# Kernel optimization log

Measured on AMD Instinct MI355X. Metric: run time of the kernel, lower is better.

Reference implementation:

```python
import jax, jax.numpy as jnp
import numpy as np

NEG_BIG = 1e13  # matches the torch module's (mask-1)*1e13 additive mask


def setup_inputs() -> dict:
    key = jax.random.key(0)
    k1, k2, k3, k4 = jax.random.split(key, 4)
    B, Lq, Lk, D = 32, 1024, 1024, 1024  # D = 2*hidden = 2*embedding
    query = jax.random.normal(k1, (B, Lq, D), dtype=jnp.float32)
    key_t = jax.random.normal(k2, (B, Lk, D), dtype=jnp.float32)
    key_mask = jax.random.randint(k3, (B, Lk), 0, 2).astype(jnp.float32)
    # Linear(hidden*2 -> embedding*2): weight [out, in] torch convention
    W = jax.random.normal(k4, (D, D), dtype=jnp.float32) * (1.0 / np.sqrt(D))
    b = jnp.zeros((D,), dtype=jnp.float32)
    return {"query": query, "key": key_t, "key_mask": key_mask, "W": W, "b": b}


def reference(query, key, key_mask, W, b):
    # query_emb: Dropout (identity at eval) -> Linear -> ReLU
    query_feat = jax.nn.relu(jnp.einsum("bqd,ed->bqe", query, W) + b)  # [B,Lq,D]
    # bmm with multiplicatively masked key
    masked_key = key * key_mask[:, :, None]                             # [B,Lk,D]
    score = jnp.einsum("bqd,bkd->bqk", query_feat, masked_key)          # [B,Lq,Lk]
    # masked_softmax: score*mask + (mask-1)*1e13, softmax over last dim
    m = key_mask[:, None, :]                                            # [B,1,Lk]
    attn = jax.nn.softmax(score * m + (m - 1.0) * NEG_BIG, axis=-1)     # [B,Lq,Lk]
    # weighted sum over the UNmasked key (as in the original module)
    return jnp.einsum("bqk,bkd->bqd", attn, key)                        # [B,Lq,D]
```

## Files before the change

### kernel.cpp

```cpp
#include <hip/hip_runtime.h>
#include <hip/hip_bf16.h>


typedef __attribute__((ext_vector_type(4))) float f32x4;
typedef __attribute__((ext_vector_type(8))) short s16x8;

#define MFMA16(a, b, c) __builtin_amdgcn_mfma_f32_16x16x32_bf16((a), (b), (c), 0, 0, 0)

__device__ __forceinline__ unsigned short f2bf(float x) {
  unsigned u = __builtin_bit_cast(unsigned, x);
  return (unsigned short)((u + 0x7FFFu + ((u >> 16) & 1u)) >> 16);
}
__device__ __forceinline__ float bf2f(unsigned short h) {
  return __builtin_bit_cast(float, ((unsigned)h) << 16);
}
__device__ __forceinline__ int swz(int row, int col) {
  return (row * 64 + col) ^ ((row & 7) << 3);
}
__device__ __forceinline__ void cvt8(const float* __restrict__ s, s16x8& h8, s16x8& l8) {
  f32x4 a = *(const f32x4*)s;
  f32x4 b = *(const f32x4*)(s + 4);
#pragma unroll
  for (int i = 0; i < 8; i++) {
    float v = (i < 4) ? a[i] : b[i - 4];
    unsigned short hu = f2bf(v);
    unsigned short lu = f2bf(v - bf2f(hu));
    h8[i] = (short)hu;
    l8[i] = (short)lu;
  }
}
__device__ __forceinline__ void gld16(const void* g, void* lds) {
  __builtin_amdgcn_global_load_lds((const __attribute__((address_space(1))) unsigned int*)g,
                                   (__attribute__((address_space(3))) unsigned int*)lds, 16, 0, 0);
}

#define OFF_KHI 0ULL
#define OFF_KLO 67108864ULL
#define OFF_KHIT 134217728ULL
#define OFF_QHI 201326592ULL
#define OFF_QLO 268435456ULL
#define OFF_WHI 335544320ULL
#define OFF_WLO 337641472ULL
#define WS_TIER_A 339738624ULL
#define WS_TIER_B2 201326592ULL

__global__ __launch_bounds__(256) void k_cvt_pair(const float* __restrict__ src,
                                                  unsigned short* __restrict__ hi,
                                                  unsigned short* __restrict__ lo, int n8) {
  int i = blockIdx.x * 256 + threadIdx.x;
  if (i >= n8) return;
  s16x8 h, l;
  cvt8(src + (size_t)i * 8, h, l);
  *(s16x8*)(hi + (size_t)i * 8) = h;
  *(s16x8*)(lo + (size_t)i * 8) = l;
}

__global__ __launch_bounds__(256) void k_cvt_k(const float* __restrict__ K,
                                               unsigned short* __restrict__ Khi,
                                               unsigned short* __restrict__ Klo,
                                               unsigned short* __restrict__ KhiT) {
  __shared__ unsigned T[64 * 65];
  const int t = threadIdx.x;
  const int db0 = blockIdx.x * 64, kb0 = blockIdx.y * 64, b = blockIdx.z;
  const size_t base = (size_t)b * 1024 * 1024;
#pragma unroll
  for (int i = 0; i < 2; i++) {
    const int r = (t >> 3) + i * 32, c0 = (t & 7) * 8;
    s16x8 h, l;
    cvt8(K + base + (size_t)(kb0 + r) * 1024 + db0 + c0, h, l);
    *(s16x8*)(Khi + base + (size_t)(kb0 + r) * 1024 + db0 + c0) = h;
    *(s16x8*)(Klo + base + (size_t)(kb0 + r) * 1024 + db0 + c0) = l;
#pragma unroll
    for (int j = 0; j < 8; j++)
      T[r * 65 + c0 + j] = ((unsigned)(unsigned short)h[j] << 16) | (unsigned short)l[j];
  }
  __syncthreads();
#pragma unroll
  for (int i = 0; i < 2; i++) {
    const int rd = (t >> 3) + i * 32, ck0 = (t & 7) * 8;
    s16x8 h;
#pragma unroll
    for (int j = 0; j < 8; j++) h[j] = (short)(unsigned short)(T[(ck0 + j) * 65 + rd] >> 16);
    *(s16x8*)(KhiT + base + (size_t)(db0 + rd) * 1024 + kb0 + ck0) = h;
  }
}

__global__ __launch_bounds__(256, 2) void k_qf2(const unsigned short* __restrict__ Qhi,
                                                const unsigned short* __restrict__ Qlo,
                                                const unsigned short* __restrict__ Whi,
                                                const unsigned short* __restrict__ Wlo,
                                                const float* __restrict__ bias,
                                                float* __restrict__ outp) {
  __shared__ __align__(16) unsigned short Ah[128 * 64], Al[128 * 64], Bh[128 * 64], Bl[128 * 64];
  const int t = threadIdx.x;
  const int i = blockIdx.x + blockIdx.y * 256;
  const int x = i & 7, j = i >> 3;
  const int n0 = (j & 7) * 128;
  const int m0 = (x * 32 + (j >> 3)) * 128;
  const int w = t >> 6, l = t & 63, wm = w >> 1, wn = w & 1, g = l >> 4, ln = l & 15;
  const int lrow = l >> 3, lc8 = (l & 7) * 8;
  const f32x4 fz = {0.f, 0.f, 0.f, 0.f};
  f32x4 acc[4][4];
#pragma unroll
  for (int a = 0; a < 4; a++)
#pragma unroll
    for (int bq = 0; bq < 4; bq++) acc[a][bq] = fz;
#pragma unroll 1
  for (int k0 = 0; k0 < 1024; k0 += 64) {
#pragma unroll
    for (int jj = 0; jj < 4; jj++) {
      const int ch = w * 4 + jj;
      const int row = ch * 8 + lrow;
      const int sc = lc8 ^ (lrow << 3);
      gld16(Qhi + (size_t)(m0 + row) * 1024 + k0 + sc, &Ah[ch * 512]);
      gld16(Qlo + (size_t)(m0 + row) * 1024 + k0 + sc, &Al[ch * 512]);
      gld16(Whi + (size_t)(n0 + row) * 1024 + k0 + sc, &Bh[ch * 512]);
      gld16(Wlo + (size_t)(n0 + row) * 1024 + k0 + sc, &Bl[ch * 512]);
    }
    __syncthreads();
#pragma unroll
    for (int ks = 0; ks < 2; ks++) {
      const int kc = ks * 32 + g * 8;
      s16x8 ah[4], al[4], bh[4], bl[4];
#pragma unroll
      for (int mf = 0; mf < 4; mf++) {
        const int row = wm * 64 + mf * 16 + ln;
        const int idx = row * 64 + (kc ^ ((row & 7) << 3));
        ah[mf] = *(const s16x8*)&Ah[idx];
        al[mf] = *(const s16x8*)&Al[idx];
      }
#pragma unroll
      for (int nf = 0; nf < 4; nf++) {
        const int row = wn * 64 + nf * 16 + ln;
        const int idx = row * 64 + (kc ^ ((row & 7) << 3));
        bh[nf] = *(const s16x8*)&Bh[idx];
        bl[nf] = *(const s16x8*)&Bl[idx];
      }
#pragma unroll
      for (int mf = 0; mf < 4; mf++)
#pragma unroll
        for (int nf = 0; nf < 4; nf++) {
          acc[mf][nf] = MFMA16(ah[mf], bh[nf], acc[mf][nf]);
          acc[mf][nf] = MFMA16(ah[mf], bl[nf], acc[mf][nf]);
          acc[mf][nf] = MFMA16(al[mf], bh[nf], acc[mf][nf]);
        }
    }
    __syncthreads();
  }
  unsigned short* oc = (unsigned short*)outp;
#pragma unroll
  for (int nf = 0; nf < 4; nf++) {
    const int col = n0 + wn * 64 + nf * 16 + ln;
    const float bv = bias[col];
#pragma unroll
    for (int mf = 0; mf < 4; mf++)
#pragma unroll
      for (int r = 0; r < 4; r++) {
        const int row = m0 + wm * 64 + mf * 16 + g * 4 + r;
        float v = acc[mf][nf][r] + bv;
        v = v > 0.f ? v : 0.f;
        unsigned short h = f2bf(v);
        oc[(size_t)row * 2048 + col] = h;
        oc[(size_t)row * 2048 + 1024 + col] = f2bf(v - bf2f(h));
      }
  }
}

__global__ __launch_bounds__(512, 2) void k_attn2(const unsigned short* __restrict__ Khi,
                                                  const unsigned short* __restrict__ Klo,
                                                  const float* __restrict__ mask,
                                                  float* __restrict__ dout) {
  __shared__ __align__(16) unsigned short kbuf[2][2][128 * 64];
  __shared__ float mask_s[1024];
  __shared__ float red[4][64];
  const int t = threadIdx.x;
  const int i = blockIdx.y * 16 + blockIdx.x;
  const int x = i & 7, jj = i >> 3;
  const int b = x * 4 + (jj >> 4), qt = jj & 15;
  const int q0 = qt * 64;
  const int w = t >> 6, l = t & 63, wm = w >> 2, wn = w & 3, g = l >> 4, ln = l & 15;
  const int lrow = l >> 3, lc8 = (l & 7) * 8, sc = lc8 ^ (lrow << 3);
  for (int ii = t; ii < 1024; ii += 512) mask_s[ii] = mask[b * 1024 + ii];
  const f32x4 fz = {0.f, 0.f, 0.f, 0.f};
  f32x4 acc[8][2][2];
#pragma unroll
  for (int kt = 0; kt < 8; kt++)
#pragma unroll
    for (int mf = 0; mf < 2; mf++)
#pragma unroll
      for (int nf = 0; nf < 2; nf++) acc[kt][mf][nf] = fz;
  const unsigned short* dou16 = (const unsigned short*)dout;
  const size_t kbase = (size_t)b * 1024 * 1024;

  auto stageK = [&](int buf, int kt, int dc) {
#pragma unroll
    for (int jj2 = 0; jj2 < 2; jj2++) {
      const int ch = w * 2 + jj2;
      const int row = ch * 8 + lrow;
      const size_t go = kbase + (size_t)(kt * 128 + row) * 1024 + dc * 64 + sc;
      gld16(Khi + go, &kbuf[buf][0][ch * 512]);
      gld16(Klo + go, &kbuf[buf][1][ch * 512]);
    }
  };

  stageK(0, 0, 0);
  __syncthreads();
  int cur = 0;
#pragma unroll 1
  for (int dc = 0; dc < 16; dc++) {
    s16x8 qh[2][2], ql[2][2];
#pragma unroll
    for (int mf = 0; mf < 2; mf++)
#pragma unroll
      for (int ks = 0; ks < 2; ks++) {
        const size_t rowoff = (size_t)(b * 1024 + q0 + wm * 32 + mf * 16 + ln) * 2048;
        const int col = dc * 64 + ks * 32 + g * 8;
        qh[mf][ks] = *(const s16x8*)(dou16 + rowoff + col);
        ql[mf][ks] = *(const s16x8*)(dou16 + rowoff + 1024 + col);
      }
#pragma unroll
    for (int kt = 0; kt < 8; kt++) {
      if (!(dc == 15 && kt == 7)) {
        const int nkt = (kt + 1) & 7;
        const int ndc = (kt == 7) ? dc + 1 : dc;
        stageK(cur ^ 1, nkt, ndc);
      }
#pragma unroll
      for (int ks = 0; ks < 2; ks++) {
        const int kc = ks * 32 + g * 8;
        s16x8 bh[2], bl[2];
#pragma unroll
        for (int nf = 0; nf < 2; nf++) {
          const int row = wn * 32 + nf * 16 + ln;
          const int idx = row * 64 + (kc ^ ((row & 7) << 3));
          bh[nf] = *(const s16x8*)&kbuf[cur][0][idx];
          bl[nf] = *(const s16x8*)&kbuf[cur][1][idx];
        }
#pragma unroll
        for (int mf = 0; mf < 2; mf++)
#pragma unroll
          for (int nf = 0; nf < 2; nf++) {
            acc[kt][mf][nf] = MFMA16(qh[mf][ks], bh[nf], acc[kt][mf][nf]);
            acc[kt][mf][nf] = MFMA16(qh[mf][ks], bl[nf], acc[kt][mf][nf]);
            acc[kt][mf][nf] = MFMA16(ql[mf][ks], bh[nf], acc[kt][mf][nf]);
          }
      }
      __syncthreads();
      cur ^= 1;
    }
  }
  float rmax[2][4];
#pragma unroll
  for (int mf = 0; mf < 2; mf++)
#pragma unroll
    for (int r = 0; r < 4; r++) rmax[mf][r] = -1e30f;
#pragma unroll
  for (int kt = 0; kt < 8; kt++)
#pragma unroll
    for (int nf = 0; nf < 2; nf++) {
      const int k = kt * 128 + wn * 32 + nf * 16 + ln;
      const bool mk = mask_s[k] != 0.f;
#pragma unroll
      for (int mf = 0; mf < 2; mf++)
#pragma unroll
        for (int r = 0; r < 4; r++)
          if (mk) rmax[mf][r] = fmaxf(rmax[mf][r], acc[kt][mf][nf][r]);
    }
#pragma unroll
  for (int off = 1; off < 16; off <<= 1)
#pragma unroll
    for (int mf = 0; mf < 2; mf++)
#pragma unroll
      for (int r = 0; r < 4; r++) rmax[mf][r] = fmaxf(rmax[mf][r], __shfl_xor(rmax[mf][r], off));
  if (ln == 0) {
#pragma unroll
    for (int mf = 0; mf < 2; mf++)
#pragma unroll
      for (int r = 0; r < 4; r++) red[wn][wm * 32 + mf * 16 + g * 4 + r] = rmax[mf][r];
  }
  __syncthreads();
#pragma unroll
  for (int mf = 0; mf < 2; mf++)
#pragma unroll
    for (int r = 0; r < 4; r++) {
      const int row = wm * 32 + mf * 16 + g * 4 + r;
      rmax[mf][r] = fmaxf(fmaxf(red[0][row], red[1][row]), fmaxf(red[2][row], red[3][row]));
    }
  __syncthreads();
  float rsum[2][4];
#pragma unroll
  for (int mf = 0; mf < 2; mf++)
#pragma unroll
    for (int r = 0; r < 4; r++) rsum[mf][r] = 0.f;
#pragma unroll
  for (int kt = 0; kt < 8; kt++)
#pragma unroll
    for (int nf = 0; nf < 2; nf++) {
      const int k = kt * 128 + wn * 32 + nf * 16 + ln;
      const bool mk = mask_s[k] != 0.f;
#pragma unroll
      for (int mf = 0; mf < 2; mf++)
#pragma unroll
        for (int r = 0; r < 4; r++)
          if (mk) rsum[mf][r] += __expf(acc[kt][mf][nf][r] - rmax[mf][r]);
    }
#pragma unroll
  for (int off = 1; off < 16; off <<= 1)
#pragma unroll
    for (int mf = 0; mf < 2; mf++)
#pragma unroll
      for (int r = 0; r < 4; r++) rsum[mf][r] += __shfl_xor(rsum[mf][r], off);
  if (ln == 0) {
#pragma unroll
    for (int mf = 0; mf < 2; mf++)
#pragma unroll
      for (int r = 0; r < 4; r++) red[wn][wm * 32 + mf * 16 + g * 4 + r] = rsum[mf][r];
  }
  __syncthreads();
  float rinv[2][4];
#pragma unroll
  for (int mf = 0; mf < 2; mf++)
#pragma unroll
    for (int r = 0; r < 4; r++) {
      const int row = wm * 32 + mf * 16 + g * 4 + r;
      rinv[mf][r] = 1.f / (red[0][row] + red[1][row] + red[2][row] + red[3][row]);
    }
  unsigned short* oc = (unsigned short*)dout;
#pragma unroll
  for (int kt = 0; kt < 8; kt++)
#pragma unroll
    for (int nf = 0; nf < 2; nf++) {
      const int k = kt * 128 + wn * 32 + nf * 16 + ln;
      const bool mk = mask_s[k] != 0.f;
#pragma unroll
      for (int mf = 0; mf < 2; mf++)
#pragma unroll
        for (int r = 0; r < 4; r++) {
          const int q = q0 + wm * 32 + mf * 16 + g * 4 + r;
          float p = mk ? __expf(acc[kt][mf][nf][r] - rmax[mf][r]) * rinv[mf][r] : 0.f;
          oc[(size_t)(b * 1024 + q) * 2048 + 1024 + k] = f2bf(p);
        }
    }
}

__global__ __launch_bounds__(512, 2) void k_pv2(const unsigned short* __restrict__ KhiT,
                                                float* __restrict__ dout, const int dh) {
  __shared__ __align__(16) unsigned short P[128 * 64];
  __shared__ __align__(16) unsigned short KT[512 * 64];
  const int t = threadIdx.x;
  const int i = blockIdx.y * 8 + blockIdx.x;
  const int x = i & 7, jj = i >> 3;
  const int b = x * 4 + (jj >> 3), qt = jj & 7;
  const int q0 = qt * 128, d0 = dh * 512;
  const int w = t >> 6, l = t & 63, wm = w >> 2, wd = w & 3, g = l >> 4, ln = l & 15;
  const int lrow = l >> 3, lc8 = (l & 7) * 8, sc = lc8 ^ (lrow << 3);
  const f32x4 fz = {0.f, 0.f, 0.f, 0.f};
  f32x4 acc[4][8];
#pragma unroll
  for (int a = 0; a < 4; a++)
#pragma unroll
    for (int bq = 0; bq < 8; bq++) acc[a][bq] = fz;
  const unsigned short* dou16 = (const unsigned short*)dout;
  const size_t kbase = (size_t)b * 1024 * 1024;
#pragma unroll 1
  for (int k0 = 0; k0 < 1024; k0 += 64) {
#pragma unroll
    for (int jj2 = 0; jj2 < 2; jj2++) {
      const int ch = w * 2 + jj2;
      const int row = ch * 8 + lrow;
      gld16(dou16 + (size_t)(b * 1024 + q0 + row) * 2048 + 1024 + k0 + sc, &P[ch * 512]);
    }
#pragma unroll
    for (int jj2 = 0; jj2 < 8; jj2++) {
      const int ch = w * 8 + jj2;
      const int row = ch * 8 + lrow;
      gld16(KhiT + kbase + (size_t)(d0 + row) * 1024 + k0 + sc, &KT[ch * 512]);
    }
    __syncthreads();
#pragma unroll
    for (int ks = 0; ks < 2; ks++) {
      const int kc = ks * 32 + g * 8;
      s16x8 a[4], bb[8];
#pragma unroll
      for (int mf = 0; mf < 4; mf++) {
        const int row = wm * 64 + mf * 16 + ln;
        a[mf] = *(const s16x8*)&P[row * 64 + (kc ^ ((row & 7) << 3))];
      }
#pragma unroll
      for (int nf = 0; nf < 8; nf++) {
        const int row = wd * 128 + nf * 16 + ln;
        bb[nf] = *(const s16x8*)&KT[row * 64 + (kc ^ ((row & 7) << 3))];
      }
#pragma unroll
      for (int mf = 0; mf < 4; mf++)
#pragma unroll
        for (int nf = 0; nf < 8; nf++) acc[mf][nf] = MFMA16(a[mf], bb[nf], acc[mf][nf]);
    }
    __syncthreads();
  }
#pragma unroll
  for (int mf = 0; mf < 4; mf++)
#pragma unroll
    for (int nf = 0; nf < 8; nf++)
#pragma unroll
      for (int r = 0; r < 4; r++) {
        const int q = q0 + wm * 64 + mf * 16 + g * 4 + r;
        const int d = d0 + wd * 128 + nf * 16 + ln;
        dout[(size_t)(b * 1024 + q) * 1024 + d] = acc[mf][nf][r];
      }
}

__global__ __launch_bounds__(256, 2) void k_qf(const float* __restrict__ Q,
                                               const float* __restrict__ W,
                                               const float* __restrict__ bias,
                                               float* __restrict__ qf, const int packout) {
  __shared__ __align__(16) short Ah[128 * 64], Al[128 * 64], Bh[128 * 64], Bl[128 * 64];
  const int t = threadIdx.x;
  const int m0 = blockIdx.x * 128, n0 = blockIdx.y * 128;
  const int w = t >> 6, l = t & 63, wm = w >> 1, wn = w & 1, g = l >> 4, ln = l & 15;
  const f32x4 fz = {0.f, 0.f, 0.f, 0.f};
  f32x4 acc[4][4];
#pragma unroll
  for (int a = 0; a < 4; a++)
#pragma unroll
    for (int bq = 0; bq < 4; bq++) acc[a][bq] = fz;
  const int srow = t >> 1, scol = (t & 1) * 32;
#pragma unroll 1
  for (int k0 = 0; k0 < 1024; k0 += 64) {
    const float* sa = Q + (size_t)(m0 + srow) * 1024 + k0 + scol;
    const float* sb = W + (size_t)(n0 + srow) * 1024 + k0 + scol;
#pragma unroll
    for (int c = 0; c < 32; c += 8) {
      s16x8 h, lo;
      cvt8(sa + c, h, lo);
      int si = swz(srow, scol + c);
      *(s16x8*)&Ah[si] = h;
      *(s16x8*)&Al[si] = lo;
    }
#pragma unroll
    for (int c = 0; c < 32; c += 8) {
      s16x8 h, lo;
      cvt8(sb + c, h, lo);
      int si = swz(srow, scol + c);
      *(s16x8*)&Bh[si] = h;
      *(s16x8*)&Bl[si] = lo;
    }
    __syncthreads();
#pragma unroll
    for (int ks = 0; ks < 2; ks++) {
      const int kc = ks * 32 + g * 8;
      s16x8 ah[4], al[4], bh[4], bl[4];
#pragma unroll
      for (int mf = 0; mf < 4; mf++) {
        int si = swz(wm * 64 + mf * 16 + ln, kc);
        ah[mf] = *(s16x8*)&Ah[si];
        al[mf] = *(s16x8*)&Al[si];
      }
#pragma unroll
      for (int nf = 0; nf < 4; nf++) {
        int si = swz(wn * 64 + nf * 16 + ln, kc);
        bh[nf] = *(s16x8*)&Bh[si];
        bl[nf] = *(s16x8*)&Bl[si];
      }
#pragma unroll
      for (int mf = 0; mf < 4; mf++)
#pragma unroll
        for (int nf = 0; nf < 4; nf++) {
          acc[mf][nf] = MFMA16(ah[mf], bh[nf], acc[mf][nf]);
          acc[mf][nf] = MFMA16(ah[mf], bl[nf], acc[mf][nf]);
          acc[mf][nf] = MFMA16(al[mf], bh[nf], acc[mf][nf]);
        }
    }
    __syncthreads();
  }
  unsigned short* oc = (unsigned short*)qf;
#pragma unroll
  for (int nf = 0; nf < 4; nf++) {
    const int col = n0 + wn * 64 + nf * 16 + ln;
    const float bv = bias[col];
#pragma unroll
    for (int mf = 0; mf < 4; mf++)
#pragma unroll
      for (int r = 0; r < 4; r++) {
        const int row = m0 + wm * 64 + mf * 16 + g * 4 + r;
        float v = acc[mf][nf][r] + bv;
        v = v > 0.f ? v : 0.f;
        if (packout) {
          unsigned short h = f2bf(v);
          oc[(size_t)row * 2048 + col] = h;
          oc[(size_t)row * 2048 + 1024 + col] = f2bf(v - bf2f(h));
        } else {
          qf[(size_t)row * 1024 + col] = v;
        }
      }
  }
}

__global__ __launch_bounds__(512, 2) void k_attn(const float* __restrict__ Key,
                                                 const float* __restrict__ mask,
                                                 float* __restrict__ dout) {
  __shared__ __align__(16) short qh[64 * 64], qlo[64 * 64], kh[128 * 64], klo[128 * 64];
  __shared__ float mask_s[1024];
  __shared__ float red[4][64];
  const int t = threadIdx.x;
  const int qt = blockIdx.x, b = blockIdx.y;
  const int q0 = qt * 64;
  const int w = t >> 6, l = t & 63, wm = w >> 2, wn = w & 3, g = l >> 4, ln = l & 15;
  for (int i = t; i < 1024; i += 512) mask_s[i] = mask[b * 1024 + i];
  const f32x4 fz = {0.f, 0.f, 0.f, 0.f};
  f32x4 acc[8][2][2];
#pragma unroll
  for (int kt = 0; kt < 8; kt++)
#pragma unroll
    for (int mf = 0; mf < 2; mf++)
#pragma unroll
      for (int nf = 0; nf < 2; nf++) acc[kt][mf][nf] = fz;
  const float* qfb = dout + (size_t)(b * 1024 + q0) * 1024;
  const float* kb = Key + (size_t)b * 1024 * 1024;
  const int qrow = t >> 3, qcol = (t & 7) * 8;
  const int krow = t >> 2, kcol0 = (t & 3) * 16;
#pragma unroll 1
  for (int dc = 0; dc < 16; dc++) {
    {
      s16x8 h, lo;
      cvt8(qfb + (size_t)qrow * 1024 + dc * 64 + qcol, h, lo);
      int si = swz(qrow, qcol);
      *(s16x8*)&qh[si] = h;
      *(s16x8*)&qlo[si] = lo;
    }
#pragma unroll
    for (int kt = 0; kt < 8; kt++) {
      {
        const float* s = kb + (size_t)(kt * 128 + krow) * 1024 + dc * 64 + kcol0;
        s16x8 h, lo;
        cvt8(s, h, lo);
        int si = swz(krow, kcol0);
        *(s16x8*)&kh[si] = h;
        *(s16x8*)&klo[si] = lo;
        cvt8(s + 8, h, lo);
        si = swz(krow, kcol0 + 8);
        *(s16x8*)&kh[si] = h;
        *(s16x8*)&klo[si] = lo;
      }
      __syncthreads();
#pragma unroll
      for (int ks = 0; ks < 2; ks++) {
        const int kc = ks * 32 + g * 8;
        s16x8 ah[2], al2[2], bh[2], bl[2];
#pragma unroll
        for (int mf = 0; mf < 2; mf++) {
          int si = swz(wm * 32 + mf * 16 + ln, kc);
          ah[mf] = *(s16x8*)&qh[si];
          al2[mf] = *(s16x8*)&qlo[si];
        }
#pragma unroll
        for (int nf = 0; nf < 2; nf++) {
          int si = swz(wn * 32 + nf * 16 + ln, kc);
          bh[nf] = *(s16x8*)&kh[si];
          bl[nf] = *(s16x8*)&klo[si];
        }
#pragma unroll
        for (int mf = 0; mf < 2; mf++)
#pragma unroll
          for (int nf = 0; nf < 2; nf++) {
            acc[kt][mf][nf] = MFMA16(ah[mf], bh[nf], acc[kt][mf][nf]);
            acc[kt][mf][nf] = MFMA16(ah[mf], bl[nf], acc[kt][mf][nf]);
            acc[kt][mf][nf] = MFMA16(al2[mf], bh[nf], acc[kt][mf][nf]);
          }
      }
      __syncthreads();
    }
  }
  float rmax[2][4];
#pragma unroll
  for (int mf = 0; mf < 2; mf++)
#pragma unroll
    for (int r = 0; r < 4; r++) rmax[mf][r] = -1e30f;
#pragma unroll
  for (int kt = 0; kt < 8; kt++)
#pragma unroll
    for (int nf = 0; nf < 2; nf++) {
      const int k = kt * 128 + wn * 32 + nf * 16 + ln;
      const bool mk = mask_s[k] != 0.f;
#pragma unroll
      for (int mf = 0; mf < 2; mf++)
#pragma unroll
        for (int r = 0; r < 4; r++)
          if (mk) rmax[mf][r] = fmaxf(rmax[mf][r], acc[kt][mf][nf][r]);
    }
#pragma unroll
  for (int off = 1; off < 16; off <<= 1)
#pragma unroll
    for (int mf = 0; mf < 2; mf++)
#pragma unroll
      for (int r = 0; r < 4; r++) rmax[mf][r] = fmaxf(rmax[mf][r], __shfl_xor(rmax[mf][r], off));
  if (ln == 0) {
#pragma unroll
    for (int mf = 0; mf < 2; mf++)
#pragma unroll
      for (int r = 0; r < 4; r++) red[wn][wm * 32 + mf * 16 + g * 4 + r] = rmax[mf][r];
  }
  __syncthreads();
#pragma unroll
  for (int mf = 0; mf < 2; mf++)
#pragma unroll
    for (int r = 0; r < 4; r++) {
      const int row = wm * 32 + mf * 16 + g * 4 + r;
      rmax[mf][r] = fmaxf(fmaxf(red[0][row], red[1][row]), fmaxf(red[2][row], red[3][row]));
    }
  __syncthreads();
  float rsum[2][4];
#pragma unroll
  for (int mf = 0; mf < 2; mf++)
#pragma unroll
    for (int r = 0; r < 4; r++) rsum[mf][r] = 0.f;
#pragma unroll
  for (int kt = 0; kt < 8; kt++)
#pragma unroll
    for (int nf = 0; nf < 2; nf++) {
      const int k = kt * 128 + wn * 32 + nf * 16 + ln;
      const bool mk = mask_s[k] != 0.f;
#pragma unroll
      for (int mf = 0; mf < 2; mf++)
#pragma unroll
        for (int r = 0; r < 4; r++)
          if (mk) rsum[mf][r] += __expf(acc[kt][mf][nf][r] - rmax[mf][r]);
    }
#pragma unroll
  for (int off = 1; off < 16; off <<= 1)
#pragma unroll
    for (int mf = 0; mf < 2; mf++)
#pragma unroll
      for (int r = 0; r < 4; r++) rsum[mf][r] += __shfl_xor(rsum[mf][r], off);
  if (ln == 0) {
#pragma unroll
    for (int mf = 0; mf < 2; mf++)
#pragma unroll
      for (int r = 0; r < 4; r++) red[wn][wm * 32 + mf * 16 + g * 4 + r] = rsum[mf][r];
  }
  __syncthreads();
  float rinv[2][4];
#pragma unroll
  for (int mf = 0; mf < 2; mf++)
#pragma unroll
    for (int r = 0; r < 4; r++) {
      const int row = wm * 32 + mf * 16 + g * 4 + r;
      rinv[mf][r] = 1.f / (red[0][row] + red[1][row] + red[2][row] + red[3][row]);
    }
  char* oc = (char*)dout;
#pragma unroll
  for (int kt = 0; kt < 8; kt++)
#pragma unroll
    for (int nf = 0; nf < 2; nf++) {
      const int k = kt * 128 + wn * 32 + nf * 16 + ln;
      const bool mk = mask_s[k] != 0.f;
#pragma unroll
      for (int mf = 0; mf < 2; mf++)
#pragma unroll
        for (int r = 0; r < 4; r++) {
          const int q = q0 + wm * 32 + mf * 16 + g * 4 + r;
          float p = mk ? __expf(acc[kt][mf][nf][r] - rmax[mf][r]) * rinv[mf][r] : 0.f;
          *(unsigned short*)(oc + (size_t)(b * 1024 + q) * 4096 + 2048 + k * 2) = f2bf(p);
        }
    }
}

__global__ __launch_bounds__(512, 2) void k_pv(const float* __restrict__ Key,
                                               float* __restrict__ dout, const int dh) {
  __shared__ __align__(16) short P[128 * 64];
  __shared__ __align__(16) short KT[512 * 64];
  const int t = threadIdx.x;
  const int qt = blockIdx.x, b = blockIdx.y;
  const int q0 = qt * 128, d0 = dh * 512;
  const int w = t >> 6, l = t & 63, wm = w >> 2, wd = w & 3, g = l >> 4, ln = l & 15;
  const f32x4 fz = {0.f, 0.f, 0.f, 0.f};
  f32x4 acc[4][8];
#pragma unroll
  for (int a = 0; a < 4; a++)
#pragma unroll
    for (int bq = 0; bq < 8; bq++) acc[a][bq] = fz;
  const char* ab = (const char*)dout;
  const int prow = t >> 2, pc0 = (t & 3) * 16;
#pragma unroll 1
  for (int k0 = 0; k0 < 1024; k0 += 64) {
    {
      const unsigned short* s =
          (const unsigned short*)(ab + (size_t)(b * 1024 + q0 + prow) * 4096 + 2048) + k0 + pc0;
      s16x8 p0 = *(const s16x8*)s, p1 = *(const s16x8*)(s + 8);
      *(s16x8*)&P[swz(prow, pc0)] = p0;
      *(s16x8*)&P[swz(prow, pc0 + 8)] = p1;
    }
    {
      const float* ksrc = Key + (size_t)b * 1024 * 1024 + (size_t)k0 * 1024 + d0 + t;
#pragma unroll
      for (int kg = 0; kg < 8; kg++) {
        s16x8 h;
#pragma unroll
        for (int jx = 0; jx < 8; jx++) h[jx] = (short)f2bf(ksrc[(size_t)(kg * 8 + jx) * 1024]);
        *(s16x8*)&KT[swz(t, kg * 8)] = h;
      }
    }
    __syncthreads();
#pragma unroll
    for (int ks = 0; ks < 2; ks++) {
      const int kc = ks * 32 + g * 8;
      s16x8 a[4], bb[8];
#pragma unroll
      for (int mf = 0; mf < 4; mf++) a[mf] = *(s16x8*)&P[swz(wm * 64 + mf * 16 + ln, kc)];
#pragma unroll
      for (int nf = 0; nf < 8; nf++) bb[nf] = *(s16x8*)&KT[swz(wd * 128 + nf * 16 + ln, kc)];
#pragma unroll
      for (int mf = 0; mf < 4; mf++)
#pragma unroll
        for (int nf = 0; nf < 8; nf++) acc[mf][nf] = MFMA16(a[mf], bb[nf], acc[mf][nf]);
    }
    __syncthreads();
  }
#pragma unroll
  for (int mf = 0; mf < 4; mf++)
#pragma unroll
    for (int nf = 0; nf < 8; nf++)
#pragma unroll
      for (int r = 0; r < 4; r++) {
        const int q = q0 + wm * 64 + mf * 16 + g * 4 + r;
        const int d = d0 + wd * 128 + nf * 16 + ln;
        dout[(size_t)(b * 1024 + q) * 1024 + d] = acc[mf][nf][r];
      }
}

extern "C" void kernel_launch(void* const* d_in, const int* in_sizes, int n_in,
                              void* d_out, int out_size, void* d_ws, size_t ws_size,
                              hipStream_t stream) {
  const float* Q = (const float*)d_in[0];
  const float* K = (const float*)d_in[1];
  const float* M = (const float*)d_in[2];
  const float* W = (const float*)d_in[3];
  const float* bias = (const float*)d_in[4];
  float* out = (float*)d_out;
  char* wsb = (char*)d_ws;
  (void)in_sizes; (void)n_in; (void)out_size;

  const bool tierA = ws_size >= WS_TIER_A;
  const bool tierB2 = !tierA && ws_size >= WS_TIER_B2;
  if (tierA || tierB2) {
    unsigned short* Khi = (unsigned short*)(wsb + OFF_KHI);
    unsigned short* Klo = (unsigned short*)(wsb + OFF_KLO);
    unsigned short* KhiT = (unsigned short*)(wsb + OFF_KHIT);
    k_cvt_k<<<dim3(16, 16, 32), 256, 0, stream>>>(K, Khi, Klo, KhiT);
    if (tierA) {
      unsigned short* Qhi = (unsigned short*)(wsb + OFF_QHI);
      unsigned short* Qlo = (unsigned short*)(wsb + OFF_QLO);
      unsigned short* Whi = (unsigned short*)(wsb + OFF_WHI);
      unsigned short* Wlo = (unsigned short*)(wsb + OFF_WLO);
      k_cvt_pair<<<16384, 256, 0, stream>>>(Q, Qhi, Qlo, 4194304);
      k_cvt_pair<<<512, 256, 0, stream>>>(W, Whi, Wlo, 131072);
      k_qf2<<<dim3(256, 8), 256, 0, stream>>>(Qhi, Qlo, Whi, Wlo, bias, out);
    } else {
      k_qf<<<dim3(256, 8), 256, 0, stream>>>(Q, W, bias, out, 1);
    }
    k_attn2<<<dim3(16, 32), 512, 0, stream>>>(Khi, Klo, M, out);
    k_pv2<<<dim3(8, 32), 512, 0, stream>>>(KhiT, out, 0);
    k_pv2<<<dim3(8, 32), 512, 0, stream>>>(KhiT, out, 1);
  } else {
    k_qf<<<dim3(256, 8), 256, 0, stream>>>(Q, W, bias, out, 0);
    k_attn<<<dim3(16, 32), 512, 0, stream>>>(K, M, out);
    k_pv<<<dim3(8, 32), 512, 0, stream>>>(K, out, 0);
    k_pv<<<dim3(8, 32), 512, 0, stream>>>(K, out, 1);
  }
}
```

Baseline: 801.0 us.

## Store query features in MFMA fragment layout and widen K staging tiles

The QF GEMM epilogue now writes the bf16 hi/lo query features in a fragment-major layout, so the attention kernel can load each lane's MFMA operand with one contiguous 16-byte read. The attention kernel stages 128-wide K chunks (twice the LDS, occupancy hint cut to 1 block per SM), which halves the outer d-loop iterations and barriers. Attention weights go to a separate workspace buffer, so the two P·V launches merge into one grid with z=2. The tier-B2 fallback is removed, and the lower occupancy may hurt latency hiding.

```diff
diff --git a/kernel.cpp b/kernel.cpp
--- a/kernel.cpp
+++ b/kernel.cpp
@@ -42,7 +42,7 @@
 #define OFF_WHI 335544320ULL
 #define OFF_WLO 337641472ULL
 #define WS_TIER_A 339738624ULL
-#define WS_TIER_B2 201326592ULL
+#define QA_LO 33554432ULL
 
 __global__ __launch_bounds__(256) void k_cvt_pair(const float* __restrict__ src,
                                                   unsigned short* __restrict__ hi,
@@ -147,30 +147,33 @@
     }
     __syncthreads();
   }
-  unsigned short* oc = (unsigned short*)outp;
+  unsigned short* qA = (unsigned short*)outp;
 #pragma unroll
   for (int nf = 0; nf < 4; nf++) {
-    const int col = n0 + wn * 64 + nf * 16 + ln;
-    const float bv = bias[col];
+    const int c = n0 + wn * 64 + nf * 16 + ln;
+    const float bv = bias[c];
+    const int kchunk = c >> 5, lhib = ((c >> 3) & 3) << 4, jj = c & 7;
 #pragma unroll
     for (int mf = 0; mf < 4; mf++)
 #pragma unroll
       for (int r = 0; r < 4; r++) {
-        const int row = m0 + wm * 64 + mf * 16 + g * 4 + r;
+        const int R = m0 + wm * 64 + mf * 16 + g * 4 + r;
         float v = acc[mf][nf][r] + bv;
         v = v > 0.f ? v : 0.f;
         unsigned short h = f2bf(v);
-        oc[(size_t)row * 2048 + col] = h;
-        oc[(size_t)row * 2048 + 1024 + col] = f2bf(v - bf2f(h));
-      }
-  }
-}
-
-__global__ __launch_bounds__(512, 2) void k_attn2(const unsigned short* __restrict__ Khi,
+        const size_t fo = (((size_t)(R >> 4) * 32 + kchunk) * 64 + ((R & 15) + lhib)) * 8 + jj;
+        qA[fo] = h;
+        qA[QA_LO + fo] = f2bf(v - bf2f(h));
+      }
+  }
+}
+
+__global__ __launch_bounds__(512, 1) void k_attn2(const unsigned short* __restrict__ Khi,
                                                   const unsigned short* __restrict__ Klo,
                                                   const float* __restrict__ mask,
-                                                  float* __restrict__ dout) {
-  __shared__ __align__(16) unsigned short kbuf[2][2][128 * 64];
+                                                  const unsigned short* __restrict__ qA,
+                                                  unsigned short* __restrict__ attnw) {
+  __shared__ __align__(16) unsigned short kbuf[2][2][128 * 128];
   __shared__ float mask_s[1024];
   __shared__ float red[4][64];
   const int t = threadIdx.x;
@@ -179,7 +182,6 @@
   const int b = x * 4 + (jj >> 4), qt = jj & 15;
   const int q0 = qt * 64;
   const int w = t >> 6, l = t & 63, wm = w >> 2, wn = w & 3, g = l >> 4, ln = l & 15;
-  const int lrow = l >> 3, lc8 = (l & 7) * 8, sc = lc8 ^ (lrow << 3);
   for (int ii = t; ii < 1024; ii += 512) mask_s[ii] = mask[b * 1024 + ii];
   const f32x4 fz = {0.f, 0.f, 0.f, 0.f};
   f32x4 acc[8][2][2];
@@ -189,15 +191,16 @@
     for (int mf = 0; mf < 2; mf++)
 #pragma unroll
       for (int nf = 0; nf < 2; nf++) acc[kt][mf][nf] = fz;
-  const unsigned short* dou16 = (const unsigned short*)dout;
   const size_t kbase = (size_t)b * 1024 * 1024;
+  const int qblk0 = (b * 1024 + q0) >> 4;
 
   auto stageK = [&](int buf, int kt, int dc) {
 #pragma unroll
-    for (int jj2 = 0; jj2 < 2; jj2++) {
-      const int ch = w * 2 + jj2;
-      const int row = ch * 8 + lrow;
-      const size_t go = kbase + (size_t)(kt * 128 + row) * 1024 + dc * 64 + sc;
+    for (int jj2 = 0; jj2 < 4; jj2++) {
+      const int ch = w * 4 + jj2;
+      const int row = ch * 4 + (l >> 4);
+      const int scc = ((l & 15) ^ (row & 7)) * 8;
+      const size_t go = kbase + (size_t)(kt * 128 + row) * 1024 + dc * 128 + scc;
       gld16(Khi + go, &kbuf[buf][0][ch * 512]);
       gld16(Klo + go, &kbuf[buf][1][ch * 512]);
     }
@@ -207,32 +210,32 @@
   __syncthreads();
   int cur = 0;
 #pragma unroll 1
-  for (int dc = 0; dc < 16; dc++) {
-    s16x8 qh[2][2], ql[2][2];
-#pragma unroll
-    for (int mf = 0; mf < 2; mf++)
-#pragma unroll
-      for (int ks = 0; ks < 2; ks++) {
-        const size_t rowoff = (size_t)(b * 1024 + q0 + wm * 32 + mf * 16 + ln) * 2048;
-        const int col = dc * 64 + ks * 32 + g * 8;
-        qh[mf][ks] = *(const s16x8*)(dou16 + rowoff + col);
-        ql[mf][ks] = *(const s16x8*)(dou16 + rowoff + 1024 + col);
-      }
+  for (int dc = 0; dc < 8; dc++) {
+    s16x8 qh[2][4], ql[2][4];
+#pragma unroll
+    for (int mf = 0; mf < 2; mf++) {
+      const int qb = qblk0 + wm * 2 + mf;
+#pragma unroll
+      for (int ks = 0; ks < 4; ks++) {
+        const size_t fo = (((size_t)qb * 32 + dc * 4 + ks) * 64 + l) * 8;
+        qh[mf][ks] = *(const s16x8*)(qA + fo);
+        ql[mf][ks] = *(const s16x8*)(qA + QA_LO + fo);
+      }
+    }
 #pragma unroll
     for (int kt = 0; kt < 8; kt++) {
-      if (!(dc == 15 && kt == 7)) {
+      if (!(dc == 7 && kt == 7)) {
         const int nkt = (kt + 1) & 7;
         const int ndc = (kt == 7) ? dc + 1 : dc;
         stageK(cur ^ 1, nkt, ndc);
       }
 #pragma unroll
-      for (int ks = 0; ks < 2; ks++) {
-        const int kc = ks * 32 + g * 8;
+      for (int ks = 0; ks < 4; ks++) {
         s16x8 bh[2], bl[2];
 #pragma unroll
         for (int nf = 0; nf < 2; nf++) {
           const int row = wn * 32 + nf * 16 + ln;
-          const int idx = row * 64 + (kc ^ ((row & 7) << 3));
+          const int idx = row * 128 + (((ks * 4 + g) ^ (row & 7)) * 8);
           bh[nf] = *(const s16x8*)&kbuf[cur][0][idx];
           bl[nf] = *(const s16x8*)&kbuf[cur][1][idx];
         }
@@ -325,7 +328,6 @@
       const int row = wm * 32 + mf * 16 + g * 4 + r;
       rinv[mf][r] = 1.f / (red[0][row] + red[1][row] + red[2][row] + red[3][row]);
     }
-  unsigned short* oc = (unsigned short*)dout;
 #pragma unroll
   for (int kt = 0; kt < 8; kt++)
 #pragma unroll
@@ -338,20 +340,21 @@
         for (int r = 0; r < 4; r++) {
           const int q = q0 + wm * 32 + mf * 16 + g * 4 + r;
           float p = mk ? __expf(acc[kt][mf][nf][r] - rmax[mf][r]) * rinv[mf][r] : 0.f;
-          oc[(size_t)(b * 1024 + q) * 2048 + 1024 + k] = f2bf(p);
+          attnw[(size_t)(b * 1024 + q) * 1024 + k] = f2bf(p);
         }
     }
 }
 
 __global__ __launch_bounds__(512, 2) void k_pv2(const unsigned short* __restrict__ KhiT,
-                                                float* __restrict__ dout, const int dh) {
+                                                const unsigned short* __restrict__ attnw,
+                                                float* __restrict__ dout) {
   __shared__ __align__(16) unsigned short P[128 * 64];
   __shared__ __align__(16) unsigned short KT[512 * 64];
   const int t = threadIdx.x;
   const int i = blockIdx.y * 8 + blockIdx.x;
   const int x = i & 7, jj = i >> 3;
   const int b = x * 4 + (jj >> 3), qt = jj & 7;
-  const int q0 = qt * 128, d0 = dh * 512;
+  const int q0 = qt * 128, d0 = blockIdx.z * 512;
   const int w = t >> 6, l = t & 63, wm = w >> 2, wd = w & 3, g = l >> 4, ln = l & 15;
   const int lrow = l >> 3, lc8 = (l & 7) * 8, sc = lc8 ^ (lrow << 3);
   const f32x4 fz = {0.f, 0.f, 0.f, 0.f};
@@ -360,7 +363,6 @@
   for (int a = 0; a < 4; a++)
 #pragma unroll
     for (int bq = 0; bq < 8; bq++) acc[a][bq] = fz;
-  const unsigned short* dou16 = (const unsigned short*)dout;
   const size_t kbase = (size_t)b * 1024 * 1024;
 #pragma unroll 1
   for (int k0 = 0; k0 < 1024; k0 += 64) {
@@ -368,7 +370,7 @@
     for (int jj2 = 0; jj2 < 2; jj2++) {
       const int ch = w * 2 + jj2;
       const int row = ch * 8 + lrow;
-      gld16(dou16 + (size_t)(b * 1024 + q0 + row) * 2048 + 1024 + k0 + sc, &P[ch * 512]);
+      gld16(attnw + (size_t)(b * 1024 + q0 + row) * 1024 + k0 + sc, &P[ch * 512]);
     }
 #pragma unroll
     for (int jj2 = 0; jj2 < 8; jj2++) {
@@ -413,7 +415,7 @@
 __global__ __launch_bounds__(256, 2) void k_qf(const float* __restrict__ Q,
                                                const float* __restrict__ W,
                                                const float* __restrict__ bias,
-                                               float* __restrict__ qf, const int packout) {
+                                               float* __restrict__ qf) {
   __shared__ __align__(16) short Ah[128 * 64], Al[128 * 64], Bh[128 * 64], Bl[128 * 64];
   const int t = threadIdx.x;
   const int m0 = blockIdx.x * 128, n0 = blockIdx.y * 128;
@@ -473,7 +475,6 @@
     }
     __syncthreads();
   }
-  unsigned short* oc = (unsigned short*)qf;
 #pragma unroll
   for (int nf = 0; nf < 4; nf++) {
     const int col = n0 + wn * 64 + nf * 16 + ln;
@@ -484,14 +485,7 @@
       for (int r = 0; r < 4; r++) {
         const int row = m0 + wm * 64 + mf * 16 + g * 4 + r;
         float v = acc[mf][nf][r] + bv;
-        v = v > 0.f ? v : 0.f;
-        if (packout) {
-          unsigned short h = f2bf(v);
-          oc[(size_t)row * 2048 + col] = h;
-          oc[(size_t)row * 2048 + 1024 + col] = f2bf(v - bf2f(h));
-        } else {
-          qf[(size_t)row * 1024 + col] = v;
-        }
+        qf[(size_t)row * 1024 + col] = v > 0.f ? v : 0.f;
       }
   }
 }
@@ -740,29 +734,23 @@
   char* wsb = (char*)d_ws;
   (void)in_sizes; (void)n_in; (void)out_size;
 
-  const bool tierA = ws_size >= WS_TIER_A;
-  const bool tierB2 = !tierA && ws_size >= WS_TIER_B2;
-  if (tierA || tierB2) {
+  if (ws_size >= WS_TIER_A) {
     unsigned short* Khi = (unsigned short*)(wsb + OFF_KHI);
     unsigned short* Klo = (unsigned short*)(wsb + OFF_KLO);
     unsigned short* KhiT = (unsigned short*)(wsb + OFF_KHIT);
+    unsigned short* Qhi = (unsigned short*)(wsb + OFF_QHI);
+    unsigned short* Qlo = (unsigned short*)(wsb + OFF_QLO);
+    unsigned short* Whi = (unsigned short*)(wsb + OFF_WHI);
+    unsigned short* Wlo = (unsigned short*)(wsb + OFF_WLO);
+    unsigned short* attnw = Qhi;
     k_cvt_k<<<dim3(16, 16, 32), 256, 0, stream>>>(K, Khi, Klo, KhiT);
-    if (tierA) {
-      unsigned short* Qhi = (unsigned short*)(wsb + OFF_QHI);
-      unsigned short* Qlo = (unsigned short*)(wsb + OFF_QLO);
-      unsigned short* Whi = (unsigned short*)(wsb + OFF_WHI);
-      unsigned short* Wlo = (unsigned short*)(wsb + OFF_WLO);
-      k_cvt_pair<<<16384, 256, 0, stream>>>(Q, Qhi, Qlo, 4194304);
-      k_cvt_pair<<<512, 256, 0, stream>>>(W, Whi, Wlo, 131072);
-      k_qf2<<<dim3(256, 8), 256, 0, stream>>>(Qhi, Qlo, Whi, Wlo, bias, out);
-    } else {
-      k_qf<<<dim3(256, 8), 256, 0, stream>>>(Q, W, bias, out, 1);
-    }
-    k_attn2<<<dim3(16, 32), 512, 0, stream>>>(Khi, Klo, M, out);
-    k_pv2<<<dim3(8, 32), 512, 0, stream>>>(KhiT, out, 0);
-    k_pv2<<<dim3(8, 32), 512, 0, stream>>>(KhiT, out, 1);
+    k_cvt_pair<<<16384, 256, 0, stream>>>(Q, Qhi, Qlo, 4194304);
+    k_cvt_pair<<<512, 256, 0, stream>>>(W, Whi, Wlo, 131072);
+    k_qf2<<<dim3(256, 8), 256, 0, stream>>>(Qhi, Qlo, Whi, Wlo, bias, out);
+    k_attn2<<<dim3(16, 32), 512, 0, stream>>>(Khi, Klo, M, (const unsigned short*)out, attnw);
+    k_pv2<<<dim3(8, 32, 2), 512, 0, stream>>>(KhiT, attnw, out);
   } else {
-    k_qf<<<dim3(256, 8), 256, 0, stream>>>(Q, W, bias, out, 0);
+    k_qf<<<dim3(256, 8), 256, 0, stream>>>(Q, W, bias, out);
     k_attn<<<dim3(16, 32), 512, 0, stream>>>(K, M, out);
     k_pv<<<dim3(8, 32), 512, 0, stream>>>(K, out, 0);
     k_pv<<<dim3(8, 32), 512, 0, stream>>>(K, out, 1);
```

After: 894.3 us. +11.7%, slower.
